# Kernel tuning notes

Measured on AMD Instinct MI355X. Metric: run time of the kernel, lower is better.

The kernel has to match this reference:

```python
import math
import jax, jax.numpy as jnp
import numpy as np

SMOOTH = 1.5
FIX_M = 30

N_LOC = 30000
N_SAMP = 32
MAX_M = 30


def setup_inputs() -> dict:
    key = jax.random.key(0)
    k1, k2, k3, k4, k5 = jax.random.split(key, 5)
    augmented_response = jax.random.normal(k1, (N_SAMP, N_LOC, MAX_M + 1), dtype=jnp.float32)
    scales = jax.random.uniform(k2, (N_LOC,), dtype=jnp.float32, minval=0.5, maxval=1.5)
    nug_mean = jax.random.uniform(k3, (N_LOC,), dtype=jnp.float32, minval=0.5, maxval=1.5)
    fraction_shrink = jax.random.uniform(k4, (1,), dtype=jnp.float32, minval=0.5, maxval=1.0)
    batch_idx = jax.random.randint(k5, (N_LOC,), 0, 100, dtype=jnp.int64 if jax.config.read('jax_enable_x64') else jnp.int32)
    # learned kernel params: theta_q, sigma_params (2,), lengthscale (log-range)
    theta_q = jnp.asarray(-1.0, dtype=jnp.float32)
    sigma_params = jnp.asarray([0.0, 0.3], dtype=jnp.float32)
    lengthscale = jnp.asarray(0.0, dtype=jnp.float32)
    return dict(augmented_response=augmented_response, scales=scales, nug_mean=nug_mean,
                fraction_shrink=fraction_shrink, batch_idx=batch_idx,
                theta_q=theta_q, sigma_params=sigma_params, lengthscale=lengthscale)


def _matern15(x):
    # x: [N, n, m] already divided by effective lengthscale; Matern nu=1.5, ls=1
    sq = jnp.sum(x * x, axis=-1)                       # [N, n]
    d2 = sq[:, :, None] + sq[:, None, :] - 2.0 * jnp.einsum('bim,bjm->bij', x, x)
    dist = jnp.sqrt(jnp.clip(d2, 0.0))                 # [N, n, n]
    s3d = math.sqrt(3.0) * dist
    return (1.0 + s3d) * jnp.exp(-s3d)


def reference(augmented_response, scales, nug_mean, fraction_shrink, batch_idx,
              theta_q, sigma_params, lengthscale):
    m = FIX_M
    x = augmented_response[..., 1:m + 1]               # [n, N, m]
    x = jnp.where(jnp.isnan(x), 0.0, x)
    x = jnp.transpose(x, (1, 0, 2))                    # [N, n, m]

    k_idx = jnp.arange(1, m + 1, dtype=x.dtype)
    scaling = jnp.exp(-0.5 * k_idx * jnp.exp(theta_q))  # [m]
    ls = jnp.exp(lengthscale) * math.sqrt(2.0 * SMOOTH)
    xl = x * (scaling / ls)                            # fused scale + lengthscale divide

    nonlinear = _matern15(xl)                          # [N, n, n]

    sigmas = jnp.exp(sigma_params[0] + sigma_params[1] * jnp.log(scales))  # [N]
    coef = fraction_shrink.reshape(()) * (sigmas * sigmas) / nug_mean      # [N]
    kmat = coef[:, None, None] * nonlinear

    eye = jnp.eye(kmat.shape[-1], dtype=kmat.dtype)
    g = kmat + eye
    g = jnp.where((batch_idx == 0)[:, None, None], eye, g)
    g_chol = jnp.linalg.cholesky(g)
    return g, g_chol, nug_mean
```

## Files before the change

### kernel.cpp

```cpp
#include <hip/hip_runtime.h>
#include <math.h>

#define NSAMP 32
#define XSTR  36
#define SQRT3 1.7320508075688772f

typedef _Float16 half8  __attribute__((ext_vector_type(8)));
typedef float    f32x16 __attribute__((ext_vector_type(16)));

__device__ __forceinline__ float rdlane(float v, int l) {
    return __int_as_float(__builtin_amdgcn_readlane(__float_as_int(v), l));
}

template<int K, int JJ>
struct Upd {
    static __device__ __forceinline__ void run(float* av, float lik) {
        av[JJ] = fmaf(-lik, rdlane(lik, JJ), av[JJ]);
        Upd<K, JJ + 1>::run(av, lik);
    }
};
template<int K>
struct Upd<K, NSAMP> { static __device__ __forceinline__ void run(float*, float) {} };

template<int K>
struct Chol {
    static __device__ __forceinline__ void run(float* av) {
        float lik = av[K] * __frsqrt_rn(rdlane(av[K], K));
        av[K] = lik;
        Upd<K, K + 1>::run(av, lik);
        Chol<K + 1>::run(av);
    }
};
template<>
struct Chol<NSAMP> { static __device__ __forceinline__ void run(float*) {} };

__global__ __launch_bounds__(256, 6) void tmk_kernel(
    const float* __restrict__ aug,
    const float* __restrict__ scales,
    const float* __restrict__ nug,
    const float* __restrict__ frac,
    const int*   __restrict__ bidx,
    const float* __restrict__ thq,
    const float* __restrict__ sigp,
    const float* __restrict__ lens,
    float* __restrict__ out,
    int n_loc)
{
    __shared__ __align__(16) float X[4][NSAMP][XSTR];
    __shared__ float SQ[4][NSAMP];

    const int tid  = threadIdx.x;
    const int w    = tid >> 6;
    const int lane = tid & 63;
    const int j    = lane & 31;
    const int hl   = lane >> 5;
    const int kb   = 8 * hl;

    const int loc0 = blockIdx.x * 4;
    int loc = loc0 + w; if (loc >= n_loc) loc = n_loc - 1;

    const size_t srow = (size_t)n_loc * 31;

    if (lane < 60) {
        const int s0 = lane / 30;
        const int k  = lane - s0 * 30;
        const float* p = aug + (size_t)s0 * srow + (size_t)loc * 31 + 1 + k;
        float* xp = &X[w][s0][k];
#pragma unroll
        for (int it = 0; it < 16; ++it) {
            float v = p[(size_t)(2 * it) * srow];
            v = (v != v) ? 0.0f : v;
            xp[2 * it * XSTR] = v;
        }
    }
    X[w][lane >> 1][30 + (lane & 1)] = 0.0f;

    const float a_s   = -0.5f * __expf(thq[0]);
    const float invls = 1.0f / (__expf(lens[0]) * SQRT3);
    float sl[8], sh[8];
#pragma unroll
    for (int e = 0; e < 8; ++e) {
        sl[e] = __expf(a_s * (float)(kb + e + 1))  * invls;
        sh[e] = __expf(a_s * (float)(kb + e + 17)) * invls;
    }

    const float* xr = &X[w][j][0];
    float4 r0 = *reinterpret_cast<const float4*>(xr + kb);
    float4 r1 = *reinterpret_cast<const float4*>(xr + kb + 4);
    float4 r2 = *reinterpret_cast<const float4*>(xr + 16 + kb);
    float4 r3 = *reinterpret_cast<const float4*>(xr + 16 + kb + 4);
    float v0[8] = {r0.x, r0.y, r0.z, r0.w, r1.x, r1.y, r1.z, r1.w};
    float v1[8] = {r2.x, r2.y, r2.z, r2.w, r3.x, r3.y, r3.z, r3.w};

    half8 fLo, fHi;
    float s0a = 0.f, s1a = 0.f;
#pragma unroll
    for (int e = 0; e < 8; ++e) {
        float a = v0[e] * sl[e];
        s0a = fmaf(a, a, s0a);
        fLo[e] = (_Float16)a;
        float b = v1[e] * sh[e];
        s1a = fmaf(b, b, s1a);
        fHi[e] = (_Float16)b;
    }
    float sqp    = s0a + s1a;
    float sqfull = sqp + __shfl_xor(sqp, 32);
    if (hl == 0) SQ[w][j] = sqfull;

    f32x16 C = {};
    C = __builtin_amdgcn_mfma_f32_32x32x16_f16(fLo, fLo, C, 0, 0, 0);
    C = __builtin_amdgcn_mfma_f32_32x32x16_f16(fHi, fHi, C, 0, 0, 0);

    const float scl = scales[loc];
    const float nm  = nug[loc];
    const float sig  = __expf(sigp[0] + sigp[1] * __logf(scl));
    const float coef = frac[0] * sig * sig / nm;
    const bool  bz   = (bidx[loc] == 0);

    float* gout = out + (size_t)loc * 1024;
    const float* sqb = &SQ[w][4 * hl];
    float av[32];
#pragma unroll
    for (int r = 0; r < 16; ++r) {
        const int row0 = (r & 3) + 8 * (r >> 2);
        const int i    = row0 + 4 * hl;
        const bool dia = (j == i);
        float sqi = sqb[row0];
        float d2  = fmaf(-2.0f, C[r], sqi + sqfull);
        d2 = dia ? 0.0f : fmaxf(d2, 0.0f);
        float s3d = __fsqrt_rn(3.0f * d2);
        float nl  = (1.0f + s3d) * __expf(-s3d);
        float dg  = dia ? 1.0f : 0.0f;
        float gv  = fmaf(coef, nl, dg);
        if (bz) gv = dg;
        gout[i * 32 + j] = gv;

        float pg = __shfl_xor(gv, 32);
        av[row0]     = hl ? pg : gv;
        av[row0 + 4] = hl ? gv : pg;
    }

    Chol<0>::run(av);

    if (lane < 32) {
        float* lrow = out + (size_t)n_loc * 1024 + (size_t)loc * 1024 + (size_t)j * 32;
#pragma unroll
        for (int c = 0; c < 8; ++c) {
            float4 wv;
            wv.x = (4 * c + 0 <= j) ? av[4 * c + 0] : 0.f;
            wv.y = (4 * c + 1 <= j) ? av[4 * c + 1] : 0.f;
            wv.z = (4 * c + 2 <= j) ? av[4 * c + 2] : 0.f;
            wv.w = (4 * c + 3 <= j) ? av[4 * c + 3] : 0.f;
            *reinterpret_cast<float4*>(&lrow[4 * c]) = wv;
        }
    }

    if (tid < 4) {
        int lc = loc0 + tid; if (lc >= n_loc) lc = n_loc - 1;
        out[(size_t)n_loc * 2048 + lc] = nug[lc];
    }
}

extern "C" void kernel_launch(void* const* d_in, const int* in_sizes, int n_in,
                              void* d_out, int out_size, void* d_ws, size_t ws_size,
                              hipStream_t stream) {
    const float* aug    = (const float*)d_in[0];
    const float* scales = (const float*)d_in[1];
    const float* nug    = (const float*)d_in[2];
    const float* frac   = (const float*)d_in[3];
    const int*   bidx   = (const int*)  d_in[4];
    const float* thq    = (const float*)d_in[5];
    const float* sigp   = (const float*)d_in[6];
    const float* lens   = (const float*)d_in[7];
    const int n_loc = in_sizes[1];

    const int nblk = (n_loc + 3) / 4;
    tmk_kernel<<<nblk, 256, 0, stream>>>(aug, scales, nug, frac, bidx, thq,
                                         sigp, lens, (float*)d_out, n_loc);
}
```

Baseline: 121.4 us.

## Pack two locations per wave and factor both Choleskys in 32-lane halves

Each wavefront now builds two Gram matrices, one after the other. The lower 32 lanes keep location A's rows and the upper 32 lanes take location B's rows, so a single register-resident Cholesky factors both at once. Previously the upper half-wave sat idle during the serial factorisation. The cross-lane broadcast changes from readlane to a ds_swizzle that broadcasts within each 32-lane group, which adds LDS-path latency on the serial diagonal dependency chain. The launch-bounds occupancy hint drops from 6 to 4 to leave more registers, and the grid now has half as many blocks.

```diff
diff --git a/kernel.cpp b/kernel.cpp
--- a/kernel.cpp
+++ b/kernel.cpp
@@ -8,14 +8,15 @@
 typedef _Float16 half8  __attribute__((ext_vector_type(8)));
 typedef float    f32x16 __attribute__((ext_vector_type(16)));
 
-__device__ __forceinline__ float rdlane(float v, int l) {
-    return __int_as_float(__builtin_amdgcn_readlane(__float_as_int(v), l));
+template<int L>
+__device__ __forceinline__ float bcast32(float v) {
+    return __int_as_float(__builtin_amdgcn_ds_swizzle(__float_as_int(v), (L << 5)));
 }
 
 template<int K, int JJ>
 struct Upd {
     static __device__ __forceinline__ void run(float* av, float lik) {
-        av[JJ] = fmaf(-lik, rdlane(lik, JJ), av[JJ]);
+        av[JJ] = fmaf(-lik, bcast32<JJ>(lik), av[JJ]);
         Upd<K, JJ + 1>::run(av, lik);
     }
 };
@@ -25,7 +26,7 @@
 template<int K>
 struct Chol {
     static __device__ __forceinline__ void run(float* av) {
-        float lik = av[K] * __frsqrt_rn(rdlane(av[K], K));
+        float lik = av[K] * __frsqrt_rn(bcast32<K>(av[K]));
         av[K] = lik;
         Upd<K, K + 1>::run(av, lik);
         Chol<K + 1>::run(av);
@@ -34,7 +35,7 @@
 template<>
 struct Chol<NSAMP> { static __device__ __forceinline__ void run(float*) {} };
 
-__global__ __launch_bounds__(256, 6) void tmk_kernel(
+__global__ __launch_bounds__(256, 4) void tmk_kernel(
     const float* __restrict__ aug,
     const float* __restrict__ scales,
     const float* __restrict__ nug,
@@ -56,15 +57,29 @@
     const int hl   = lane >> 5;
     const int kb   = 8 * hl;
 
-    const int loc0 = blockIdx.x * 4;
-    int loc = loc0 + w; if (loc >= n_loc) loc = n_loc - 1;
+    const int locA = blockIdx.x * 8 + w * 2;
+    int locB = locA + 1; if (locB >= n_loc) locB = n_loc - 1;
 
     const size_t srow = (size_t)n_loc * 31;
+
+    const float a_s   = -0.5f * __expf(thq[0]);
+    const float invls = 1.0f / (__expf(lens[0]) * SQRT3);
+    float sl[8], sh[8];
+#pragma unroll
+    for (int e = 0; e < 8; ++e) {
+        sl[e] = __expf(a_s * (float)(kb + e + 1))  * invls;
+        sh[e] = __expf(a_s * (float)(kb + e + 17)) * invls;
+    }
+    const float fr = frac[0], sp0 = sigp[0], sp1 = sigp[1];
+
+    X[w][lane >> 1][30 + (lane & 1)] = 0.0f;
+
+    float av[32];
 
     if (lane < 60) {
         const int s0 = lane / 30;
         const int k  = lane - s0 * 30;
-        const float* p = aug + (size_t)s0 * srow + (size_t)loc * 31 + 1 + k;
+        const float* p = aug + (size_t)s0 * srow + (size_t)locA * 31 + 1 + k;
         float* xp = &X[w][s0][k];
 #pragma unroll
         for (int it = 0; it < 16; ++it) {
@@ -73,77 +88,137 @@
             xp[2 * it * XSTR] = v;
         }
     }
-    X[w][lane >> 1][30 + (lane & 1)] = 0.0f;
-
-    const float a_s   = -0.5f * __expf(thq[0]);
-    const float invls = 1.0f / (__expf(lens[0]) * SQRT3);
-    float sl[8], sh[8];
-#pragma unroll
-    for (int e = 0; e < 8; ++e) {
-        sl[e] = __expf(a_s * (float)(kb + e + 1))  * invls;
-        sh[e] = __expf(a_s * (float)(kb + e + 17)) * invls;
-    }
-
-    const float* xr = &X[w][j][0];
-    float4 r0 = *reinterpret_cast<const float4*>(xr + kb);
-    float4 r1 = *reinterpret_cast<const float4*>(xr + kb + 4);
-    float4 r2 = *reinterpret_cast<const float4*>(xr + 16 + kb);
-    float4 r3 = *reinterpret_cast<const float4*>(xr + 16 + kb + 4);
-    float v0[8] = {r0.x, r0.y, r0.z, r0.w, r1.x, r1.y, r1.z, r1.w};
-    float v1[8] = {r2.x, r2.y, r2.z, r2.w, r3.x, r3.y, r3.z, r3.w};
-
-    half8 fLo, fHi;
-    float s0a = 0.f, s1a = 0.f;
-#pragma unroll
-    for (int e = 0; e < 8; ++e) {
-        float a = v0[e] * sl[e];
-        s0a = fmaf(a, a, s0a);
-        fLo[e] = (_Float16)a;
-        float b = v1[e] * sh[e];
-        s1a = fmaf(b, b, s1a);
-        fHi[e] = (_Float16)b;
-    }
-    float sqp    = s0a + s1a;
-    float sqfull = sqp + __shfl_xor(sqp, 32);
-    if (hl == 0) SQ[w][j] = sqfull;
-
-    f32x16 C = {};
-    C = __builtin_amdgcn_mfma_f32_32x32x16_f16(fLo, fLo, C, 0, 0, 0);
-    C = __builtin_amdgcn_mfma_f32_32x32x16_f16(fHi, fHi, C, 0, 0, 0);
-
-    const float scl = scales[loc];
-    const float nm  = nug[loc];
-    const float sig  = __expf(sigp[0] + sigp[1] * __logf(scl));
-    const float coef = frac[0] * sig * sig / nm;
-    const bool  bz   = (bidx[loc] == 0);
-
-    float* gout = out + (size_t)loc * 1024;
-    const float* sqb = &SQ[w][4 * hl];
-    float av[32];
-#pragma unroll
-    for (int r = 0; r < 16; ++r) {
-        const int row0 = (r & 3) + 8 * (r >> 2);
-        const int i    = row0 + 4 * hl;
-        const bool dia = (j == i);
-        float sqi = sqb[row0];
-        float d2  = fmaf(-2.0f, C[r], sqi + sqfull);
-        d2 = dia ? 0.0f : fmaxf(d2, 0.0f);
-        float s3d = __fsqrt_rn(3.0f * d2);
-        float nl  = (1.0f + s3d) * __expf(-s3d);
-        float dg  = dia ? 1.0f : 0.0f;
-        float gv  = fmaf(coef, nl, dg);
-        if (bz) gv = dg;
-        gout[i * 32 + j] = gv;
-
-        float pg = __shfl_xor(gv, 32);
-        av[row0]     = hl ? pg : gv;
-        av[row0 + 4] = hl ? gv : pg;
+    {
+        const float* xr = &X[w][j][0];
+        float4 r0 = *reinterpret_cast<const float4*>(xr + kb);
+        float4 r1 = *reinterpret_cast<const float4*>(xr + kb + 4);
+        float4 r2 = *reinterpret_cast<const float4*>(xr + 16 + kb);
+        float4 r3 = *reinterpret_cast<const float4*>(xr + 16 + kb + 4);
+        float v0[8] = {r0.x, r0.y, r0.z, r0.w, r1.x, r1.y, r1.z, r1.w};
+        float v1[8] = {r2.x, r2.y, r2.z, r2.w, r3.x, r3.y, r3.z, r3.w};
+
+        half8 fLoA, fHiA;
+        float s0a = 0.f, s1a = 0.f;
+#pragma unroll
+        for (int e = 0; e < 8; ++e) {
+            float a = v0[e] * sl[e];
+            s0a = fmaf(a, a, s0a);
+            fLoA[e] = (_Float16)a;
+            float b = v1[e] * sh[e];
+            s1a = fmaf(b, b, s1a);
+            fHiA[e] = (_Float16)b;
+        }
+        float sqp     = s0a + s1a;
+        float sqfullA = sqp + __shfl_xor(sqp, 32);
+        if (hl == 0) SQ[w][j] = sqfullA;
+
+        f32x16 C1 = {};
+        C1 = __builtin_amdgcn_mfma_f32_32x32x16_f16(fLoA, fLoA, C1, 0, 0, 0);
+        C1 = __builtin_amdgcn_mfma_f32_32x32x16_f16(fHiA, fHiA, C1, 0, 0, 0);
+
+        const float sclA = scales[locA];
+        const float sigA = __expf(sp0 + sp1 * __logf(sclA));
+        const float coefA = fr * sigA * sigA / nug[locA];
+        const bool  bzA   = (bidx[locA] == 0);
+
+        float* goutA = out + (size_t)locA * 1024;
+        const float* sqb = &SQ[w][4 * hl];
+#pragma unroll
+        for (int r = 0; r < 16; ++r) {
+            const int row0 = (r & 3) + 8 * (r >> 2);
+            const int i    = row0 + 4 * hl;
+            const bool dia = (j == i);
+            float sqi = sqb[row0];
+            float d2  = fmaf(-2.0f, C1[r], sqi + sqfullA);
+            d2 = dia ? 0.0f : fmaxf(d2, 0.0f);
+            float s3d = __fsqrt_rn(3.0f * d2);
+            float nl  = (1.0f + s3d) * __expf(-s3d);
+            float dg  = dia ? 1.0f : 0.0f;
+            float gv  = fmaf(coefA, nl, dg);
+            if (bzA) gv = dg;
+            goutA[i * 32 + j] = gv;
+
+            float pg = __shfl_xor(gv, 32);
+            av[row0]     = hl ? pg : gv;
+            av[row0 + 4] = hl ? gv : pg;
+        }
+    }
+
+    __builtin_amdgcn_sched_barrier(0x20);
+
+    if (lane < 60) {
+        const int s0 = lane / 30;
+        const int k  = lane - s0 * 30;
+        const float* p = aug + (size_t)s0 * srow + (size_t)locB * 31 + 1 + k;
+        float* xp = &X[w][s0][k];
+#pragma unroll
+        for (int it = 0; it < 16; ++it) {
+            float v = p[(size_t)(2 * it) * srow];
+            v = (v != v) ? 0.0f : v;
+            xp[2 * it * XSTR] = v;
+        }
+    }
+    {
+        const float* xr = &X[w][j][0];
+        float4 r0 = *reinterpret_cast<const float4*>(xr + kb);
+        float4 r1 = *reinterpret_cast<const float4*>(xr + kb + 4);
+        float4 r2 = *reinterpret_cast<const float4*>(xr + 16 + kb);
+        float4 r3 = *reinterpret_cast<const float4*>(xr + 16 + kb + 4);
+        float v0[8] = {r0.x, r0.y, r0.z, r0.w, r1.x, r1.y, r1.z, r1.w};
+        float v1[8] = {r2.x, r2.y, r2.z, r2.w, r3.x, r3.y, r3.z, r3.w};
+
+        half8 fLoB, fHiB;
+        float s0a = 0.f, s1a = 0.f;
+#pragma unroll
+        for (int e = 0; e < 8; ++e) {
+            float a = v0[e] * sl[e];
+            s0a = fmaf(a, a, s0a);
+            fLoB[e] = (_Float16)a;
+            float b = v1[e] * sh[e];
+            s1a = fmaf(b, b, s1a);
+            fHiB[e] = (_Float16)b;
+        }
+        float sqp     = s0a + s1a;
+        float sqfullB = sqp + __shfl_xor(sqp, 32);
+        if (hl == 0) SQ[w][j] = sqfullB;
+
+        f32x16 C2 = {};
+        C2 = __builtin_amdgcn_mfma_f32_32x32x16_f16(fLoB, fLoB, C2, 0, 0, 0);
+        C2 = __builtin_amdgcn_mfma_f32_32x32x16_f16(fHiB, fHiB, C2, 0, 0, 0);
+
+        const float sclB = scales[locB];
+        const float sigB = __expf(sp0 + sp1 * __logf(sclB));
+        const float coefB = fr * sigB * sigB / nug[locB];
+        const bool  bzB   = (bidx[locB] == 0);
+
+        float* goutB = out + (size_t)locB * 1024;
+        const float* sqb = &SQ[w][4 * hl];
+#pragma unroll
+        for (int r = 0; r < 16; ++r) {
+            const int row0 = (r & 3) + 8 * (r >> 2);
+            const int i    = row0 + 4 * hl;
+            const bool dia = (j == i);
+            float sqi = sqb[row0];
+            float d2  = fmaf(-2.0f, C2[r], sqi + sqfullB);
+            d2 = dia ? 0.0f : fmaxf(d2, 0.0f);
+            float s3d = __fsqrt_rn(3.0f * d2);
+            float nl  = (1.0f + s3d) * __expf(-s3d);
+            float dg  = dia ? 1.0f : 0.0f;
+            float gv  = fmaf(coefB, nl, dg);
+            if (bzB) gv = dg;
+            goutB[i * 32 + j] = gv;
+
+            float pg = __shfl_xor(gv, 32);
+            av[row0]     = hl ? pg : av[row0];
+            av[row0 + 4] = hl ? gv : av[row0 + 4];
+        }
     }
 
     Chol<0>::run(av);
 
-    if (lane < 32) {
-        float* lrow = out + (size_t)n_loc * 1024 + (size_t)loc * 1024 + (size_t)j * 32;
+    {
+        const int locS = hl ? locB : locA;
+        float* lrow = out + (size_t)n_loc * 1024 + (size_t)locS * 1024 + (size_t)j * 32;
 #pragma unroll
         for (int c = 0; c < 8; ++c) {
             float4 wv;
@@ -155,8 +230,8 @@
         }
     }
 
-    if (tid < 4) {
-        int lc = loc0 + tid; if (lc >= n_loc) lc = n_loc - 1;
+    if (tid < 8) {
+        int lc = blockIdx.x * 8 + tid; if (lc >= n_loc) lc = n_loc - 1;
         out[(size_t)n_loc * 2048 + lc] = nug[lc];
     }
 }
@@ -174,7 +249,7 @@
     const float* lens   = (const float*)d_in[7];
     const int n_loc = in_sizes[1];
 
-    const int nblk = (n_loc + 3) / 4;
+    const int nblk = (n_loc + 7) / 8;
     tmk_kernel<<<nblk, 256, 0, stream>>>(aug, scales, nug, frac, bidx, thq,
                                          sigp, lens, (float*)d_out, n_loc);
 }
```

New measurement: 131.4 us. 1.08x slower.

## Split fused kernel into separate Gram-matrix and Cholesky kernels

Applied to the files above, without the earlier changes.

Splits the single fused kernel into two launches. The first builds the Gram matrix G and writes it out. The second reads G back from global memory and runs the register-level Cholesky. The scaling-factor exponentials are also moved ahead of the global loads. The split is meant to lower register pressure and the cross-lane shuffles in each kernel, at the cost of an extra 123 MB round trip through memory (a re-read of G) and a second launch.

```diff
diff --git a/kernel.cpp b/kernel.cpp
--- a/kernel.cpp
+++ b/kernel.cpp
@@ -34,7 +34,7 @@
 template<>
 struct Chol<NSAMP> { static __device__ __forceinline__ void run(float*) {} };
 
-__global__ __launch_bounds__(256, 6) void tmk_kernel(
+__global__ __launch_bounds__(256, 6) void g_kernel(
     const float* __restrict__ aug,
     const float* __restrict__ scales,
     const float* __restrict__ nug,
@@ -61,6 +61,15 @@
 
     const size_t srow = (size_t)n_loc * 31;
 
+    const float a_s   = -0.5f * __expf(thq[0]);
+    const float invls = 1.0f / (__expf(lens[0]) * SQRT3);
+    float sl[8], sh[8];
+#pragma unroll
+    for (int e = 0; e < 8; ++e) {
+        sl[e] = __expf(a_s * (float)(kb + e + 1))  * invls;
+        sh[e] = __expf(a_s * (float)(kb + e + 17)) * invls;
+    }
+
     if (lane < 60) {
         const int s0 = lane / 30;
         const int k  = lane - s0 * 30;
@@ -74,15 +83,6 @@
         }
     }
     X[w][lane >> 1][30 + (lane & 1)] = 0.0f;
-
-    const float a_s   = -0.5f * __expf(thq[0]);
-    const float invls = 1.0f / (__expf(lens[0]) * SQRT3);
-    float sl[8], sh[8];
-#pragma unroll
-    for (int e = 0; e < 8; ++e) {
-        sl[e] = __expf(a_s * (float)(kb + e + 1))  * invls;
-        sh[e] = __expf(a_s * (float)(kb + e + 17)) * invls;
-    }
 
     const float* xr = &X[w][j][0];
     float4 r0 = *reinterpret_cast<const float4*>(xr + kb);
@@ -119,7 +119,6 @@
 
     float* gout = out + (size_t)loc * 1024;
     const float* sqb = &SQ[w][4 * hl];
-    float av[32];
 #pragma unroll
     for (int r = 0; r < 16; ++r) {
         const int row0 = (r & 3) + 8 * (r >> 2);
@@ -134,16 +133,39 @@
         float gv  = fmaf(coef, nl, dg);
         if (bz) gv = dg;
         gout[i * 32 + j] = gv;
-
-        float pg = __shfl_xor(gv, 32);
-        av[row0]     = hl ? pg : gv;
-        av[row0 + 4] = hl ? gv : pg;
+    }
+
+    if (tid < 4) {
+        int lc = loc0 + tid; if (lc >= n_loc) lc = n_loc - 1;
+        out[(size_t)n_loc * 2048 + lc] = nug[lc];
+    }
+}
+
+__global__ __launch_bounds__(256, 6) void chol_kernel(
+    const float* __restrict__ g,
+    float* __restrict__ lout,
+    int n_loc)
+{
+    const int tid  = threadIdx.x;
+    const int w    = tid >> 6;
+    const int lane = tid & 63;
+    const int j    = lane & 31;
+
+    int loc = blockIdx.x * 4 + w; if (loc >= n_loc) loc = n_loc - 1;
+
+    const float* grow = g + (size_t)loc * 1024 + (size_t)j * 32;
+    float av[32];
+#pragma unroll
+    for (int c = 0; c < 8; ++c) {
+        float4 v = *reinterpret_cast<const float4*>(grow + 4 * c);
+        av[4 * c + 0] = v.x; av[4 * c + 1] = v.y;
+        av[4 * c + 2] = v.z; av[4 * c + 3] = v.w;
     }
 
     Chol<0>::run(av);
 
     if (lane < 32) {
-        float* lrow = out + (size_t)n_loc * 1024 + (size_t)loc * 1024 + (size_t)j * 32;
+        float* lrow = lout + (size_t)loc * 1024 + (size_t)j * 32;
 #pragma unroll
         for (int c = 0; c < 8; ++c) {
             float4 wv;
@@ -153,11 +175,6 @@
             wv.w = (4 * c + 3 <= j) ? av[4 * c + 3] : 0.f;
             *reinterpret_cast<float4*>(&lrow[4 * c]) = wv;
         }
-    }
-
-    if (tid < 4) {
-        int lc = loc0 + tid; if (lc >= n_loc) lc = n_loc - 1;
-        out[(size_t)n_loc * 2048 + lc] = nug[lc];
     }
 }
 
@@ -174,7 +191,10 @@
     const float* lens   = (const float*)d_in[7];
     const int n_loc = in_sizes[1];
 
+    float* out = (float*)d_out;
     const int nblk = (n_loc + 3) / 4;
-    tmk_kernel<<<nblk, 256, 0, stream>>>(aug, scales, nug, frac, bidx, thq,
-                                         sigp, lens, (float*)d_out, n_loc);
-}
+
+    g_kernel<<<nblk, 256, 0, stream>>>(aug, scales, nug, frac, bidx, thq,
+                                       sigp, lens, out, n_loc);
+    chol_kernel<<<nblk, 256, 0, stream>>>(out, out + (size_t)n_loc * 1024, n_loc);
+}
```

New measurement: 117.8 us. 3.0% less time.
